# Kernel tuning notes

Measured on AMD Instinct MI355X. Metric: run time of the kernel, lower is better.

The kernel has to match this reference:

```python
import jax, jax.numpy as jnp
import numpy as np

B = 8192
ITEM_NUM = 10000


def setup_inputs() -> dict:
    key = jax.random.key(0)
    k1, k2, k3, k4, k5, k6 = jax.random.split(key, 6)
    hidden_states = jax.random.normal(k1, (B, ITEM_NUM), dtype=jnp.float32)
    targetQs_s = jax.random.normal(k2, (B, ITEM_NUM), dtype=jnp.float32)
    rewards = jax.random.uniform(k3, (B,), dtype=jnp.float32)
    actions = jax.random.randint(k4, (B,), 0, ITEM_NUM)
    is_done = jnp.zeros((B,), dtype=bool)
    discount = jnp.ones((), dtype=jnp.float32) * 0.99
    # fc = nn.Linear(item_num, 1): weight [1, item_num], bias [1]
    bound = 1.0 / np.sqrt(ITEM_NUM)
    W = jax.random.uniform(k5, (1, ITEM_NUM), minval=-bound, maxval=bound, dtype=jnp.float32)
    b = jax.random.uniform(k6, (1,), minval=-bound, maxval=bound, dtype=jnp.float32)
    return {
        "hidden_states": hidden_states,
        "actions": actions,
        "rewards": rewards,
        "discount": discount,
        "targetQs_s": targetQs_s,
        "is_done": is_done,
        "W": W,
        "b": b,
    }


def reference(hidden_states, actions, rewards, discount, targetQs_s, is_done, W, b):
    # Batched equivalent of the per-sample loop:
    # q_i = relu(fc(state_i)); nq_i = relu(fc(next_state_i))
    # loss_i = |reward_i + discount * nq_i - q_i| for non-done samples
    q = jax.nn.relu(jnp.einsum('bi,oi->bo', hidden_states, W) + b)[:, 0]   # [B]
    nq = jax.nn.relu(jnp.einsum('bi,oi->bo', targetQs_s, W) + b)[:, 0]     # [B]
    per_sample = jnp.abs(rewards + discount * nq - q)                      # [B]
    total = jnp.sum(jnp.where(is_done, jnp.float32(0.0), per_sample))
    return total / hidden_states.shape[0]
```

## Files before the change

### kernel.cpp

```cpp
#include <hip/hip_runtime.h>

#define ROWS 8192
#define COLS 10000
#define COLS4 (COLS / 4)
#define BLK 256

__global__ __launch_bounds__(BLK) void qloss_rows_kernel(
    const float* __restrict__ hidden,
    const float* __restrict__ target,
    const float* __restrict__ rewards,
    const float* __restrict__ discount,
    const unsigned char* __restrict__ is_done,
    const float* __restrict__ W,
    const float* __restrict__ bias,
    float* __restrict__ partial)
{
    const int row = blockIdx.x;
    const float4* __restrict__ h4 = (const float4*)(hidden + (size_t)row * COLS);
    const float4* __restrict__ t4 = (const float4*)(target + (size_t)row * COLS);
    const float4* __restrict__ w4 = (const float4*)W;

    float ah = 0.f, at = 0.f;
    for (int j = threadIdx.x; j < COLS4; j += BLK) {
        float4 w = w4[j];
        float4 h = h4[j];
        float4 t = t4[j];
        ah += h.x * w.x + h.y * w.y + h.z * w.z + h.w * w.w;
        at += t.x * w.x + t.y * w.y + t.z * w.z + t.w * w.w;
    }

    #pragma unroll
    for (int off = 32; off > 0; off >>= 1) {
        ah += __shfl_down(ah, off, 64);
        at += __shfl_down(at, off, 64);
    }

    __shared__ float sh[BLK / 64], st[BLK / 64];
    const int lane = threadIdx.x & 63;
    const int wid  = threadIdx.x >> 6;
    if (lane == 0) { sh[wid] = ah; st[wid] = at; }
    __syncthreads();

    if (threadIdx.x == 0) {
        float dh = sh[0] + sh[1] + sh[2] + sh[3];
        float dt = st[0] + st[1] + st[2] + st[3];
        float b  = bias[0];
        float q  = fmaxf(dh + b, 0.f);
        float nq = fmaxf(dt + b, 0.f);
        float loss = fabsf(rewards[row] + discount[0] * nq - q);
        partial[row] = is_done[row] ? 0.f : loss;
    }
}

__global__ __launch_bounds__(BLK) void qloss_reduce_kernel(
    const float* __restrict__ partial,
    float* __restrict__ out)
{
    float s = 0.f;
    for (int i = threadIdx.x; i < ROWS; i += BLK) s += partial[i];

    #pragma unroll
    for (int off = 32; off > 0; off >>= 1) s += __shfl_down(s, off, 64);

    __shared__ float sm[BLK / 64];
    const int lane = threadIdx.x & 63;
    const int wid  = threadIdx.x >> 6;
    if (lane == 0) sm[wid] = s;
    __syncthreads();

    if (threadIdx.x == 0) {
        float total = sm[0] + sm[1] + sm[2] + sm[3];
        out[0] = total / (float)ROWS;
    }
}

extern "C" void kernel_launch(void* const* d_in, const int* in_sizes, int n_in,
                              void* d_out, int out_size, void* d_ws, size_t ws_size,
                              hipStream_t stream) {
    const float*         hidden   = (const float*)d_in[0];
    const float*         rewards  = (const float*)d_in[2];
    const float*         discount = (const float*)d_in[3];
    const float*         target   = (const float*)d_in[4];
    const unsigned char* is_done  = (const unsigned char*)d_in[5];
    const float*         W        = (const float*)d_in[6];
    const float*         b        = (const float*)d_in[7];
    float*               out      = (float*)d_out;
    float*               partial  = (float*)d_ws;

    qloss_rows_kernel<<<ROWS, BLK, 0, stream>>>(
        hidden, target, rewards, discount, is_done, W, b, partial);
    qloss_reduce_kernel<<<1, BLK, 0, stream>>>(partial, out);
}
```

Measured before the change: 621.8 us.

## Assign one wavefront per row with unrolled nontemporal loads

Each 64-lane wavefront now computes one row's two dot products, so a 256-thread block handles four rows and the shared-memory cross-wave reduction and __syncthreads are removed. The inner loop is unrolled by two with independent accumulators to keep more loads in flight. The streaming hidden and target reads use nontemporal loads to avoid polluting the cache. Each wave makes more loop iterations per row, and memory-level parallelism then depends on the unroll and on occupancy.

```diff
diff --git a/kernel.cpp b/kernel.cpp
--- a/kernel.cpp
+++ b/kernel.cpp
@@ -4,6 +4,13 @@
 #define COLS 10000
 #define COLS4 (COLS / 4)
 #define BLK 256
+#define WAVES_PER_BLK (BLK / 64)
+
+typedef float vf4 __attribute__((ext_vector_type(4)));
+
+__device__ __forceinline__ float dot4(vf4 a, vf4 b) {
+    return a.x * b.x + a.y * b.y + a.z * b.z + a.w * b.w;
+}
 
 __global__ __launch_bounds__(BLK) void qloss_rows_kernel(
     const float* __restrict__ hidden,
@@ -15,19 +22,38 @@
     const float* __restrict__ bias,
     float* __restrict__ partial)
 {
-    const int row = blockIdx.x;
-    const float4* __restrict__ h4 = (const float4*)(hidden + (size_t)row * COLS);
-    const float4* __restrict__ t4 = (const float4*)(target + (size_t)row * COLS);
-    const float4* __restrict__ w4 = (const float4*)W;
+    const int lane = threadIdx.x & 63;
+    const int wid  = threadIdx.x >> 6;
+    const int row  = blockIdx.x * WAVES_PER_BLK + wid;
 
-    float ah = 0.f, at = 0.f;
-    for (int j = threadIdx.x; j < COLS4; j += BLK) {
-        float4 w = w4[j];
-        float4 h = h4[j];
-        float4 t = t4[j];
-        ah += h.x * w.x + h.y * w.y + h.z * w.z + h.w * w.w;
-        at += t.x * w.x + t.y * w.y + t.z * w.z + t.w * w.w;
+    const vf4* __restrict__ h4 = (const vf4*)(hidden + (size_t)row * COLS);
+    const vf4* __restrict__ t4 = (const vf4*)(target + (size_t)row * COLS);
+    const vf4* __restrict__ w4 = (const vf4*)W;
+
+    float ah0 = 0.f, ah1 = 0.f, at0 = 0.f, at1 = 0.f;
+    int j = lane;
+    for (; j + 64 < COLS4; j += 128) {
+        vf4 w0 = w4[j];
+        vf4 w1 = w4[j + 64];
+        vf4 h0 = __builtin_nontemporal_load(&h4[j]);
+        vf4 h1 = __builtin_nontemporal_load(&h4[j + 64]);
+        vf4 t0 = __builtin_nontemporal_load(&t4[j]);
+        vf4 t1 = __builtin_nontemporal_load(&t4[j + 64]);
+        ah0 += dot4(h0, w0);
+        ah1 += dot4(h1, w1);
+        at0 += dot4(t0, w0);
+        at1 += dot4(t1, w1);
     }
+    if (j < COLS4) {
+        vf4 w0 = w4[j];
+        vf4 h0 = __builtin_nontemporal_load(&h4[j]);
+        vf4 t0 = __builtin_nontemporal_load(&t4[j]);
+        ah0 += dot4(h0, w0);
+        at0 += dot4(t0, w0);
+    }
+
+    float ah = ah0 + ah1;
+    float at = at0 + at1;
 
     #pragma unroll
     for (int off = 32; off > 0; off >>= 1) {
@@ -35,18 +61,10 @@
         at += __shfl_down(at, off, 64);
     }
 
-    __shared__ float sh[BLK / 64], st[BLK / 64];
-    const int lane = threadIdx.x & 63;
-    const int wid  = threadIdx.x >> 6;
-    if (lane == 0) { sh[wid] = ah; st[wid] = at; }
-    __syncthreads();
-
-    if (threadIdx.x == 0) {
-        float dh = sh[0] + sh[1] + sh[2] + sh[3];
-        float dt = st[0] + st[1] + st[2] + st[3];
+    if (lane == 0) {
         float b  = bias[0];
-        float q  = fmaxf(dh + b, 0.f);
-        float nq = fmaxf(dt + b, 0.f);
+        float q  = fmaxf(ah + b, 0.f);
+        float nq = fmaxf(at + b, 0.f);
         float loss = fabsf(rewards[row] + discount[0] * nq - q);
         partial[row] = is_done[row] ? 0.f : loss;
     }
@@ -87,7 +105,7 @@
     float*               out      = (float*)d_out;
     float*               partial  = (float*)d_ws;
 
-    qloss_rows_kernel<<<ROWS, BLK, 0, stream>>>(
+    qloss_rows_kernel<<<ROWS / WAVES_PER_BLK, BLK, 0, stream>>>(
         hidden, target, rewards, discount, is_done, W, b, partial);
     qloss_reduce_kernel<<<1, BLK, 0, stream>>>(partial, out);
 }
```

Result: faster. 586.6 us (-5.7%).
